# Performance work log

Hardware: AMD Instinct MI355X
Metric: run time of the kernel (lower is better)

Reference implementation:

```python
import jax, jax.numpy as jnp
import numpy as np

L = 5        # num_layers
D = 128      # emb_dim
H = 2 * D    # mlp hidden
N_ATOM_FEATS, ATOM_VOCAB = 9, 120
N_BOND_FEATS, BOND_VOCAB = 3, 6
BN_EPS = 1e-5


def setup_inputs() -> dict:
    key = jax.random.key(0)
    ks = jax.random.split(key, 16)
    N, E = 200000, 400000
    x = jax.random.randint(ks[0], (N, N_ATOM_FEATS), 0, ATOM_VOCAB)
    edge_index = jax.random.randint(ks[1], (2, E), 0, N)
    edge_attr = jax.random.randint(ks[2], (E, N_BOND_FEATS), 0, BOND_VOCAB)
    s = 0.02
    return {
        "x": x,
        "edge_index": edge_index,
        "edge_attr": edge_attr,
        "atom_emb": jax.random.normal(ks[3], (N_ATOM_FEATS, ATOM_VOCAB, D), jnp.float32) * s,
        "bond_emb": jax.random.normal(ks[4], (L, N_BOND_FEATS, BOND_VOCAB, D), jnp.float32) * s,
        "W1": jax.random.normal(ks[5], (L, D, H), jnp.float32) * s,
        "b1": jnp.zeros((L, H), jnp.float32),
        "bn1_g": jnp.ones((L, H), jnp.float32),
        "bn1_b": jnp.zeros((L, H), jnp.float32),
        "W2": jax.random.normal(ks[6], (L, H, D), jnp.float32) * s,
        "b2": jnp.zeros((L, D), jnp.float32),
        "eps": jnp.zeros((L,), jnp.float32),
        "out_bn_g": jnp.ones((L, D), jnp.float32),
        "out_bn_b": jnp.zeros((L, D), jnp.float32),
    }


def _batchnorm(z, g, b):
    mu = jnp.mean(z, axis=0, keepdims=True)
    var = jnp.var(z, axis=0, keepdims=True)
    return (z - mu) * jax.lax.rsqrt(var + BN_EPS) * g + b


def _multi_embed(tables, idx):
    # tables: [F, V, D], idx: [N, F] -> sum_f tables[f][idx[:, f]] : [N, D]
    gathered = jax.vmap(lambda tab, i: tab[i], in_axes=(0, 1))(tables, idx)  # [F, N, D]
    return jnp.sum(gathered, axis=0)


def reference(x, edge_index, edge_attr, atom_emb, bond_emb, W1, b1, bn1_g, bn1_b,
              W2, b2, eps, out_bn_g, out_bn_b):
    N = x.shape[0]
    src, dst = edge_index[0], edge_index[1]
    h = _multi_embed(atom_emb, x)  # AtomEncoder: [N, D]
    for l in range(L):
        e = _multi_embed(bond_emb[l], edge_attr)          # BondEncoder: [E, D]
        msg = jax.nn.relu(h[src] + e)                     # message
        aggr = jax.ops.segment_sum(msg, dst, num_segments=N)  # scatter-add
        z = (1.0 + eps[l]) * h + aggr                     # GIN combine
        z = jax.nn.relu(_batchnorm(z @ W1[l] + b1[l], bn1_g[l], bn1_b[l]))
        z = z @ W2[l] + b2[l]
        h = jax.nn.relu(_batchnorm(z, out_bn_g[l], out_bn_b[l]))  # relu+dropout(p=0)
    return h  # JK='last'
```

## Files before the change

kernel.cpp:

```cpp
#include <hip/hip_runtime.h>

#define NF_ATOM 9
#define NF_BOND 3
#define DD 128
#define HH 256
#define NLAYER 5
#define NSHARD 32
#define NCODE 216
#define GRAM_NB 256

typedef float fv4 __attribute__((ext_vector_type(4)));
typedef __bf16 bfv8 __attribute__((ext_vector_type(8)));
typedef unsigned int uv4 __attribute__((ext_vector_type(4)));

__device__ inline unsigned short f2bf(float f) {
    unsigned int u = __builtin_bit_cast(unsigned int, f);
    u = u + 0x7FFFu + ((u >> 16) & 1u);
    return (unsigned short)(u >> 16);
}
__device__ inline float bf2f(unsigned short s) {
    unsigned int u = ((unsigned int)s) << 16;
    return __builtin_bit_cast(float, u);
}

__global__ __launch_bounds__(256) void k_atom(const int* __restrict__ x,
        const float* __restrict__ emb, unsigned short* __restrict__ h, int N) {
    int gid = blockIdx.x * 256 + threadIdx.x;
    int n = gid >> 5;
    if (n >= N) return;
    int c = (gid & 31) << 2;
    const int* xr = x + n * NF_ATOM;
    float4 acc = make_float4(0.f, 0.f, 0.f, 0.f);
#pragma unroll
    for (int f = 0; f < NF_ATOM; ++f) {
        int idx = xr[f];
        float4 v = *(const float4*)(emb + ((size_t)(f * 120 + idx) * DD) + c);
        acc.x += v.x; acc.y += v.y; acc.z += v.z; acc.w += v.w;
    }
    ushort4 o;
    o.x = f2bf(acc.x); o.y = f2bf(acc.y); o.z = f2bf(acc.z); o.w = f2bf(acc.w);
    *(ushort4*)(h + (size_t)n * DD + c) = o;
}

__global__ __launch_bounds__(256) void k_wconv(const float* __restrict__ W1,
        const float* __restrict__ W2, unsigned short* __restrict__ W1t,
        unsigned short* __restrict__ W2t) {
    int id = blockIdx.x * 256 + threadIdx.x;
    const int T1 = NLAYER * 4 * 256 * 32;
    if (id < T1) {
        int k = id & 31, n = (id >> 5) & 255, kc = (id >> 13) & 3, l = id >> 15;
        int o = id & 32767;
        float w = W1[((size_t)(l * 128 + kc * 32 + k)) * 256 + n];
        unsigned short hi = f2bf(w);
        W1t[(size_t)l * 65536 + o] = hi;
        W1t[(size_t)l * 65536 + 32768 + o] = f2bf(w - bf2f(hi));
    } else {
        int id2 = id - T1;
        if (id2 >= NLAYER * 8 * 128 * 32) return;
        int k = id2 & 31, n = (id2 >> 5) & 127, kc = (id2 >> 12) & 7, l = id2 >> 15;
        int o = id2 & 32767;
        float w = W2[((size_t)(l * 256 + kc * 32 + k)) * 128 + n];
        unsigned short hi = f2bf(w);
        W2t[(size_t)l * 65536 + o] = hi;
        W2t[(size_t)l * 65536 + 32768 + o] = f2bf(w - bf2f(hi));
    }
}

__global__ __launch_bounds__(256) void k_bsumtab(const float* __restrict__ bemb,
        float* __restrict__ tab) {
    int id = blockIdx.x * 256 + threadIdx.x;
    if (id >= NLAYER * NCODE * DD) return;
    int c = id & 127;
    int code = (id >> 7) % NCODE;
    int l = id / (NCODE * DD);
    int a0 = code % 6, a1 = (code / 6) % 6, a2 = code / 36;
    const float* bl = bemb + (size_t)l * NF_BOND * 6 * DD;
    tab[id] = bl[(0 * 6 + a0) * DD + c] + bl[(1 * 6 + a1) * DD + c] + bl[(2 * 6 + a2) * DD + c];
}

__global__ __launch_bounds__(256) void k_deg(const int* __restrict__ ei, int* __restrict__ deg, int E) {
    int e = blockIdx.x * 256 + threadIdx.x;
    if (e < E) atomicAdd(&deg[ei[E + e]], 1);
}
__global__ __launch_bounds__(256) void k_bsum(const int* __restrict__ deg, int* __restrict__ bsum, int N) {
    __shared__ int red[256];
    int t = threadIdx.x, b = blockIdx.x;
    int i0 = b * 1024 + t * 4;
    int s = 0;
#pragma unroll
    for (int j = 0; j < 4; ++j) if (i0 + j < N) s += deg[i0 + j];
    red[t] = s; __syncthreads();
    for (int off = 128; off > 0; off >>= 1) {
        if (t < off) red[t] += red[t + off];
        __syncthreads();
    }
    if (t == 0) bsum[b] = red[0];
}
__global__ __launch_bounds__(256) void k_bscan(const int* __restrict__ bsum, int* __restrict__ boff, int nb) {
    __shared__ int ts[256];
    int t = threadIdx.x;
    int v = (t < nb) ? bsum[t] : 0;
    ts[t] = v; __syncthreads();
    for (int off = 1; off < 256; off <<= 1) {
        int u = (t >= off) ? ts[t - off] : 0;
        __syncthreads();
        ts[t] += u;
        __syncthreads();
    }
    if (t < nb) boff[t] = ts[t] - v;
}
__global__ __launch_bounds__(256) void k_csr(const int* deg, const int* __restrict__ boff,
        int* rs, int N, int E) {
    __shared__ int ts[256];
    int t = threadIdx.x, b = blockIdx.x;
    int i0 = b * 1024 + t * 4;
    int d[4];
#pragma unroll
    for (int j = 0; j < 4; ++j) d[j] = (i0 + j < N) ? deg[i0 + j] : 0;
    int tsum = d[0] + d[1] + d[2] + d[3];
    ts[t] = tsum; __syncthreads();
    for (int off = 1; off < 256; off <<= 1) {
        int u = (t >= off) ? ts[t - off] : 0;
        __syncthreads();
        ts[t] += u;
        __syncthreads();
    }
    int base = boff[b] + ts[t] - tsum;
    int p = 0;
#pragma unroll
    for (int j = 0; j < 4; ++j) {
        int dj = d[j];
        if (i0 + j < N) rs[i0 + j] = base + p;
        p += dj;
    }
    if (b == 0 && t == 0) rs[N] = E;
}
__global__ __launch_bounds__(256) void k_scatter(const int* __restrict__ ei,
        const int* __restrict__ ea, int* __restrict__ rs, int* __restrict__ epack, int E) {
    int e = blockIdx.x * 256 + threadIdx.x;
    if (e < E) {
        int pos = atomicAdd(&rs[ei[E + e]], 1);
        int code = ea[e * 3 + 0] + 6 * ea[e * 3 + 1] + 36 * ea[e * 3 + 2];
        epack[pos] = ei[e] | (code << 18);
    }
}

__global__ void k_red(const float* __restrict__ sh, int C, const float* __restrict__ bng,
        const float* __restrict__ bnb, float invN,
        float* __restrict__ sc_out, float* __restrict__ sh_out) {
    int t = threadIdx.x;
    if (t >= C) return;
    float a = 0.f, qq = 0.f;
#pragma unroll
    for (int s = 0; s < NSHARD; ++s) {
        a += sh[s * 2 * C + t];
        qq += sh[s * 2 * C + C + t];
    }
    float mu = a * invN;
    float var = qq * invN - mu * mu;
    float r = rsqrtf(var + 1e-5f);
    float sc = bng[t] * r;
    sc_out[t] = sc; sh_out[t] = bnb[t] - mu * sc;
}

__device__ inline void edge_acc(ushort4 hv, float4 bv, float4 sc, float4 sh, int mode, float* ag) {
    float h0 = bf2f(hv.x), h1 = bf2f(hv.y), h2 = bf2f(hv.z), h3 = bf2f(hv.w);
    if (mode) {
        h0 = fmaxf(h0 * sc.x + sh.x, 0.f); h1 = fmaxf(h1 * sc.y + sh.y, 0.f);
        h2 = fmaxf(h2 * sc.z + sh.z, 0.f); h3 = fmaxf(h3 * sc.w + sh.w, 0.f);
    }
    ag[0] += fmaxf(h0 + bv.x, 0.f); ag[1] += fmaxf(h1 + bv.y, 0.f);
    ag[2] += fmaxf(h2 + bv.z, 0.f); ag[3] += fmaxf(h3 + bv.w, 0.f);
}

__global__ __launch_bounds__(256) void k_zbuild(const unsigned short* __restrict__ y2h,
        const int* __restrict__ rs, const int* __restrict__ epack,
        const float* __restrict__ btab, const float* __restrict__ sctab,
        const float* __restrict__ shtab, const float* __restrict__ epsv,
        int l, int mode, unsigned short* __restrict__ z, int N) {
    int gid = blockIdx.x * 256 + threadIdx.x;
    int n = gid >> 5;
    if (n >= N) return;
    int c = (gid & 31) << 2;
    float4 sc4 = make_float4(1.f, 1.f, 1.f, 1.f), sh4 = make_float4(0.f, 0.f, 0.f, 0.f);
    if (mode) { sc4 = *(const float4*)(sctab + c); sh4 = *(const float4*)(shtab + c); }
    int p0 = (n == 0) ? 0 : rs[n - 1];
    int p1 = rs[n];
    float ag[4] = {0.f, 0.f, 0.f, 0.f};
    int p = p0;
    for (; p + 2 <= p1; p += 2) {
        int rec0 = epack[p], rec1 = epack[p + 1];
        int s0 = rec0 & 0x3FFFF, s1 = rec1 & 0x3FFFF;
        int c0 = ((unsigned int)rec0) >> 18, c1 = ((unsigned int)rec1) >> 18;
        ushort4 h0 = *(const ushort4*)(y2h + (size_t)s0 * DD + c);
        ushort4 h1 = *(const ushort4*)(y2h + (size_t)s1 * DD + c);
        float4 b0 = *(const float4*)(btab + (size_t)c0 * DD + c);
        float4 b1 = *(const float4*)(btab + (size_t)c1 * DD + c);
        edge_acc(h0, b0, sc4, sh4, mode, ag);
        edge_acc(h1, b1, sc4, sh4, mode, ag);
    }
    if (p < p1) {
        int rec = epack[p];
        int s0 = rec & 0x3FFFF;
        int c0 = ((unsigned int)rec) >> 18;
        ushort4 h0 = *(const ushort4*)(y2h + (size_t)s0 * DD + c);
        float4 b0 = *(const float4*)(btab + (size_t)c0 * DD + c);
        edge_acc(h0, b0, sc4, sh4, mode, ag);
    }
    float ep = 1.0f + epsv[l];
    ushort4 sv = *(const ushort4*)(y2h + (size_t)n * DD + c);
    float hz[4] = {bf2f(sv.x), bf2f(sv.y), bf2f(sv.z), bf2f(sv.w)};
    if (mode) {
        hz[0] = fmaxf(hz[0] * sc4.x + sh4.x, 0.f);
        hz[1] = fmaxf(hz[1] * sc4.y + sh4.y, 0.f);
        hz[2] = fmaxf(hz[2] * sc4.z + sh4.z, 0.f);
        hz[3] = fmaxf(hz[3] * sc4.w + sh4.w, 0.f);
    }
    ushort4 o;
    o.x = f2bf(ep * hz[0] + ag[0]);
    o.y = f2bf(ep * hz[1] + ag[1]);
    o.z = f2bf(ep * hz[2] + ag[2]);
    o.w = f2bf(ep * hz[3] + ag[3]);
    *(ushort4*)(z + (size_t)n * DD + c) = o;
}

__global__ __launch_bounds__(256) void k_gram(const unsigned short* __restrict__ z,
        float* __restrict__ shardG, float* __restrict__ csS, int N) {
    __shared__ uv4 zT[128 * 8];
    int tid = threadIdx.x;
    int lane = tid & 63, wave = tid >> 6, lq = lane >> 4, lr = lane & 15;
    int cg = tid & 15;
    float cs[8] = {0, 0, 0, 0, 0, 0, 0, 0};
    fv4 acc[2][8];
#pragma unroll
    for (int ti = 0; ti < 2; ++ti)
#pragma unroll
        for (int tj = 0; tj < 8; ++tj) acc[ti][tj] = (fv4){0.f, 0.f, 0.f, 0.f};

    int ntile = N >> 6;
    for (int t = blockIdx.x; t < ntile; t += GRAM_NB) {
        const unsigned short* zt0 = z + ((size_t)t << 6) * DD;
        __syncthreads();
#pragma unroll
        for (int i = 0; i < 2; ++i) {
            int rp = i * 16 + (tid >> 4);
            int r0 = rp * 2;
            uv4 a = *(const uv4*)(zt0 + (size_t)r0 * DD + cg * 8);
            uv4 b = *(const uv4*)(zt0 + (size_t)(r0 + 1) * DD + cg * 8);
            int g = rp >> 2;
            int eo = rp & 3;
#pragma unroll
            for (int j = 0; j < 4; ++j) {
                unsigned int lo0 = a[j] & 0xFFFFu, hi0 = a[j] >> 16;
                unsigned int lo1 = b[j] & 0xFFFFu, hi1 = b[j] >> 16;
                cs[2 * j] += bf2f((unsigned short)lo0) + bf2f((unsigned short)lo1);
                cs[2 * j + 1] += bf2f((unsigned short)hi0) + bf2f((unsigned short)hi1);
                int ch0 = cg * 8 + 2 * j, ch1 = ch0 + 1;
                int s0 = ch0 * 8 + (g ^ ((ch0 ^ (ch0 >> 3)) & 7));
                int s1 = ch1 * 8 + (g ^ ((ch1 ^ (ch1 >> 3)) & 7));
                ((unsigned int*)zT)[s0 * 4 + eo] = lo0 | (lo1 << 16);
                ((unsigned int*)zT)[s1 * 4 + eo] = hi0 | (hi1 << 16);
            }
        }
        __syncthreads();
#pragma unroll
        for (int ks = 0; ks < 2; ++ks) {
            bfv8 af[2], bfr[8];
#pragma unroll
            for (int ti = 0; ti < 2; ++ti) {
                int ch = wave * 32 + ti * 16 + lr;
                af[ti] = __builtin_bit_cast(bfv8, zT[ch * 8 + ((ks * 4 + lq) ^ ((ch ^ (ch >> 3)) & 7))]);
            }
#pragma unroll
            for (int tj = 0; tj < 8; ++tj) {
                int ch = tj * 16 + lr;
                bfr[tj] = __builtin_bit_cast(bfv8, zT[ch * 8 + ((ks * 4 + lq) ^ ((ch ^ (ch >> 3)) & 7))]);
            }
#pragma unroll
            for (int ti = 0; ti < 2; ++ti)
#pragma unroll
                for (int tj = 0; tj < 8; ++tj)
                    acc[ti][tj] = __builtin_amdgcn_mfma_f32_16x16x32_bf16(af[ti], bfr[tj], acc[ti][tj], 0, 0, 0);
        }
    }
    float* gsh = shardG + (size_t)blockIdx.x * (DD * DD);
#pragma unroll
    for (int ti = 0; ti < 2; ++ti) {
        int gi = wave * 32 + ti * 16 + lq * 4;
#pragma unroll
        for (int tj = 0; tj < 8; ++tj) {
            int gj = tj * 16 + lr;
#pragma unroll
            for (int r = 0; r < 4; ++r)
                gsh[(size_t)(gi + r) * DD + gj] = acc[ti][tj][r];
        }
    }
    __syncthreads();
    float* red = (float*)zT;
#pragma unroll
    for (int j = 0; j < 8; ++j) red[tid * 8 + j] = cs[j];
    __syncthreads();
    if (tid < 128) {
        int cgg = tid >> 3, j = tid & 7;
        float a = 0.f;
#pragma unroll
        for (int k = 0; k < 16; ++k) a += red[(k * 16 + cgg) * 8 + j];
        csS[blockIdx.x * DD + cgg * 8 + j] = a;
    }
}

__global__ __launch_bounds__(256) void k_gred(const float* __restrict__ shardG,
        const float* __restrict__ csS, float* __restrict__ G, float* __restrict__ cs) {
    int idx = blockIdx.x * 256 + threadIdx.x;
    if (idx < DD * DD) {
        float a = 0.f;
#pragma unroll 8
        for (int s = 0; s < GRAM_NB; ++s) a += shardG[(size_t)s * DD * DD + idx];
        G[idx] = a;
    } else if (idx < DD * DD + DD) {
        int t = idx - DD * DD;
        float a = 0.f;
#pragma unroll 8
        for (int s = 0; s < GRAM_NB; ++s) a += csS[s * DD + t];
        cs[t] = a;
    }
}

__global__ __launch_bounds__(128) void k_redG(const float* __restrict__ G,
        const float* __restrict__ cs, const unsigned short* __restrict__ W1l,
        const float* __restrict__ b1, const float* __restrict__ bng,
        const float* __restrict__ bnb, float invN,
        float* __restrict__ sc_out, float* __restrict__ sh_out) {
    __shared__ float wv[128];
    __shared__ float redA[128], redB[128];
    int j = blockIdx.x;
    int t = threadIdx.x;
    int kc = t >> 5, kk = t & 31;
    int o = kc * 8192 + j * 32 + kk;
    float w_t = bf2f(W1l[o]) + bf2f(W1l[32768 + o]);
    wv[t] = w_t;
    __syncthreads();
    const float4* Gr = (const float4*)(G + (size_t)t * DD);
    float d = 0.f;
#pragma unroll
    for (int i = 0; i < 32; ++i) {
        float4 g4 = Gr[i];
        d += g4.x * wv[i * 4] + g4.y * wv[i * 4 + 1] + g4.z * wv[i * 4 + 2] + g4.w * wv[i * 4 + 3];
    }
    redA[t] = w_t * d;
    redB[t] = cs[t] * w_t;
    __syncthreads();
    for (int off = 64; off > 0; off >>= 1) {
        if (t < off) { redA[t] += redA[t + off]; redB[t] += redB[t + off]; }
        __syncthreads();
    }
    if (t == 0) {
        float bj = b1[j];
        float csw = redB[0];
        float mean = csw * invN + bj;
        float ey2 = redA[0] * invN + 2.f * bj * csw * invN + bj * bj;
        float var = ey2 - mean * mean;
        float r = rsqrtf(var + 1e-5f);
        float sc = bng[j] * r;
        sc_out[j] = sc;
        sh_out[j] = bnb[j] - mean * sc + bj * sc;
    }
}

__global__ __launch_bounds__(256) void k_fgemm(const unsigned short* __restrict__ z,
        const unsigned short* __restrict__ W1l, const unsigned short* __restrict__ W2l,
        const float* __restrict__ sc1, const float* __restrict__ sh1,
        const float* __restrict__ bias2,
        unsigned short* __restrict__ y2h, float* __restrict__ shard, int N) {
    __shared__ uv4 smem[3072];
    uv4* zt = smem;
    uv4* wt = smem + 1024;
    uv4* at = smem;
    uv4* wt2 = smem + 2048;
    int tid = threadIdx.x;
    int row0 = blockIdx.x * 64;
    int wave = tid >> 6, lane = tid & 63, lq = lane >> 4, lr = lane & 15;
    int rbase = tid >> 4, gz = tid & 15;

    uv4 zr[4];
#pragma unroll
    for (int i = 0; i < 4; ++i)
        zr[i] = *(const uv4*)(z + (size_t)(row0 + i * 16 + rbase) * DD + gz * 8);
    const uv4* w1src = (const uv4*)W1l;
    uv4 wrh[4], wrl[4];
#pragma unroll
    for (int i = 0; i < 4; ++i) {
        wrh[i] = w1src[i * 256 + tid];
        wrl[i] = w1src[4096 + i * 256 + tid];
    }
#pragma unroll
    for (int i = 0; i < 4; ++i) {
        int row = i * 16 + rbase;
        zt[row * 16 + (gz ^ (row & 15))] = zr[i];
    }

    fv4 acc1[4][4];
#pragma unroll
    for (int mc = 0; mc < 4; ++mc)
#pragma unroll
        for (int nr = 0; nr < 4; ++nr) acc1[mc][nr] = (fv4){0.f, 0.f, 0.f, 0.f};

    for (int kc = 0; kc < 4; ++kc) {
        __syncthreads();
#pragma unroll
        for (int i = 0; i < 4; ++i) {
            int g = i * 256 + tid;
            int wn = g >> 2, gw = g & 3;
            int slot = wn * 4 + (gw ^ ((wn >> 1) & 3));
            wt[slot] = wrh[i];
            wt[1024 + slot] = wrl[i];
        }
        __syncthreads();
        if (kc < 3) {
#pragma unroll
            for (int i = 0; i < 4; ++i) {
                wrh[i] = w1src[(size_t)(kc + 1) * 1024 + i * 256 + tid];
                wrl[i] = w1src[4096 + (size_t)(kc + 1) * 1024 + i * 256 + tid];
            }
        }
        bfv8 wfh[4], wfl[4], zf[4];
#pragma unroll
        for (int mc = 0; mc < 4; ++mc) {
            int col = wave * 64 + mc * 16 + lr;
            int slot = col * 4 + (lq ^ ((col >> 1) & 3));
            wfh[mc] = __builtin_bit_cast(bfv8, wt[slot]);
            wfl[mc] = __builtin_bit_cast(bfv8, wt[1024 + slot]);
        }
#pragma unroll
        for (int nr = 0; nr < 4; ++nr) {
            int row = nr * 16 + lr;
            zf[nr] = __builtin_bit_cast(bfv8, zt[row * 16 + ((kc * 4 + lq) ^ (row & 15))]);
        }
#pragma unroll
        for (int mc = 0; mc < 4; ++mc)
#pragma unroll
            for (int nr = 0; nr < 4; ++nr) {
                acc1[mc][nr] = __builtin_amdgcn_mfma_f32_16x16x32_bf16(wfh[mc], zf[nr], acc1[mc][nr], 0, 0, 0);
                acc1[mc][nr] = __builtin_amdgcn_mfma_f32_16x16x32_bf16(wfl[mc], zf[nr], acc1[mc][nr], 0, 0, 0);
            }
    }
    __syncthreads();

    const uv4* w2src = (const uv4*)W2l;
    uv4 wr2h[2], wr2l[2];
    wr2h[0] = w2src[tid]; wr2h[1] = w2src[256 + tid];
    wr2l[0] = w2src[4096 + tid]; wr2l[1] = w2src[4096 + 256 + tid];

#pragma unroll
    for (int mc = 0; mc < 4; ++mc) {
        int ycol0 = wave * 64 + mc * 16 + lq * 4;
        float4 s4 = *(const float4*)(sc1 + ycol0);
        float4 h4 = *(const float4*)(sh1 + ycol0);
        int gg = wave * 8 + mc * 2 + (lq >> 1);
#pragma unroll
        for (int nr = 0; nr < 4; ++nr) {
            int zrow = nr * 16 + lr;
            float v0 = fmaxf(acc1[mc][nr][0] * s4.x + h4.x, 0.f);
            float v1 = fmaxf(acc1[mc][nr][1] * s4.y + h4.y, 0.f);
            float v2 = fmaxf(acc1[mc][nr][2] * s4.z + h4.z, 0.f);
            float v3 = fmaxf(acc1[mc][nr][3] * s4.w + h4.w, 0.f);
            uint2 pk;
            pk.x = (unsigned int)f2bf(v0) | ((unsigned int)f2bf(v1) << 16);
            pk.y = (unsigned int)f2bf(v2) | ((unsigned int)f2bf(v3) << 16);
            int gs = gg ^ (zrow & 15);
            ((uint2*)at)[(zrow * 32 + gs) * 2 + (lq & 1)] = pk;
        }
    }

    fv4 acc2[4][2];
#pragma unroll
    for (int m = 0; m < 4; ++m) { acc2[m][0] = (fv4){0.f,0.f,0.f,0.f}; acc2[m][1] = (fv4){0.f,0.f,0.f,0.f}; }

    for (int kc = 0; kc < 8; ++kc) {
        __syncthreads();
        {
            int wn = tid >> 2, gw = tid & 3;
            int slot = wn * 4 + (gw ^ ((wn >> 1) & 3));
            wt2[slot] = wr2h[0];
            wt2[512 + slot] = wr2l[0];
            int g3 = 256 + tid, wn3 = g3 >> 2, gw3 = g3 & 3;
            int slot3 = wn3 * 4 + (gw3 ^ ((wn3 >> 1) & 3));
            wt2[slot3] = wr2h[1];
            wt2[512 + slot3] = wr2l[1];
        }
        __syncthreads();
        if (kc < 7) {
            wr2h[0] = w2src[(size_t)(kc + 1) * 512 + tid];
            wr2h[1] = w2src[(size_t)(kc + 1) * 512 + 256 + tid];
            wr2l[0] = w2src[4096 + (size_t)(kc + 1) * 512 + tid];
            wr2l[1] = w2src[4096 + (size_t)(kc + 1) * 512 + 256 + tid];
        }
        bfv8 a[4], bh[2], bl[2];
#pragma unroll
        for (int m = 0; m < 4; ++m) {
            int row = m * 16 + lr;
            a[m] = __builtin_bit_cast(bfv8, at[row * 32 + ((kc * 4 + lq) ^ (row & 15))]);
        }
#pragma unroll
        for (int nb = 0; nb < 2; ++nb) {
            int col = wave * 32 + nb * 16 + lr;
            int slot = col * 4 + (lq ^ ((col >> 1) & 3));
            bh[nb] = __builtin_bit_cast(bfv8, wt2[slot]);
            bl[nb] = __builtin_bit_cast(bfv8, wt2[512 + slot]);
        }
#pragma unroll
        for (int m = 0; m < 4; ++m)
#pragma unroll
            for (int nb = 0; nb < 2; ++nb) {
                acc2[m][nb] = __builtin_amdgcn_mfma_f32_16x16x32_bf16(a[m], bh[nb], acc2[m][nb], 0, 0, 0);
                acc2[m][nb] = __builtin_amdgcn_mfma_f32_16x16x32_bf16(a[m], bl[nb], acc2[m][nb], 0, 0, 0);
            }
    }

    float bv[2], s[2], q[2];
#pragma unroll
    for (int nb = 0; nb < 2; ++nb) {
        bv[nb] = bias2[wave * 32 + nb * 16 + lr];
        s[nb] = 0.f; q[nb] = 0.f;
    }
#pragma unroll
    for (int m = 0; m < 4; ++m)
#pragma unroll
        for (int nb = 0; nb < 2; ++nb) {
            int col = wave * 32 + nb * 16 + lr;
#pragma unroll
            for (int r = 0; r < 4; ++r) {
                float v = acc2[m][nb][r] + bv[nb];
                unsigned short ub = f2bf(v);
                float vr = bf2f(ub);
                int row = row0 + m * 16 + lq * 4 + r;
                y2h[(size_t)row * DD + col] = ub;
                s[nb] += vr; q[nb] += vr * vr;
            }
        }
#pragma unroll
    for (int nb = 0; nb < 2; ++nb) {
        s[nb] += __shfl_xor(s[nb], 16); s[nb] += __shfl_xor(s[nb], 32);
        q[nb] += __shfl_xor(q[nb], 16); q[nb] += __shfl_xor(q[nb], 32);
    }
    if (lane < 16) {
        int shb = (blockIdx.x & (NSHARD - 1)) * 256;
#pragma unroll
        for (int nb = 0; nb < 2; ++nb) {
            int col = wave * 32 + nb * 16 + lr;
            atomicAdd(shard + shb + col, s[nb]);
            atomicAdd(shard + shb + 128 + col, q[nb]);
        }
    }
}

__global__ __launch_bounds__(256) void k_bnfinal(const unsigned short* __restrict__ y2h,
        const float* __restrict__ sc2, const float* __restrict__ sh2,
        float* __restrict__ out, int N) {
    size_t base = ((size_t)blockIdx.x * 256 + threadIdx.x) * 4;
    if (base >= (size_t)N * DD) return;
    int c = (int)(base & (DD - 1));
    ushort4 v = *(const ushort4*)(y2h + base);
    float4 s = *(const float4*)(sc2 + c);
    float4 t = *(const float4*)(sh2 + c);
    float4 o;
    o.x = fmaxf(bf2f(v.x) * s.x + t.x, 0.f);
    o.y = fmaxf(bf2f(v.y) * s.y + t.y, 0.f);
    o.z = fmaxf(bf2f(v.z) * s.z + t.z, 0.f);
    o.w = fmaxf(bf2f(v.w) * s.w + t.w, 0.f);
    *(float4*)(out + base) = o;
}

extern "C" void kernel_launch(void* const* d_in, const int* in_sizes, int n_in,
                              void* d_out, int out_size, void* d_ws, size_t ws_size,
                              hipStream_t stream) {
    const int* x = (const int*)d_in[0];
    const int* ei = (const int*)d_in[1];
    const int* ea = (const int*)d_in[2];
    const float* atom_emb = (const float*)d_in[3];
    const float* bond_emb = (const float*)d_in[4];
    const float* W1 = (const float*)d_in[5];
    const float* b1 = (const float*)d_in[6];
    const float* bn1_g = (const float*)d_in[7];
    const float* bn1_b = (const float*)d_in[8];
    const float* W2 = (const float*)d_in[9];
    const float* b2 = (const float*)d_in[10];
    const float* epsv = (const float*)d_in[11];
    const float* obn_g = (const float*)d_in[12];
    const float* obn_b = (const float*)d_in[13];
    int N = in_sizes[0] / NF_ATOM;
    int E = in_sizes[1] / 2;

    char* wsb = (char*)d_ws;
    unsigned short* y2h = (unsigned short*)wsb;
    unsigned short* zb = (unsigned short*)(wsb + (size_t)N * 256);
    int* epack = (int*)(wsb + (size_t)N * 512);
    unsigned short* w1t = (unsigned short*)(wsb + (size_t)N * 512 + (size_t)E * 4);
    unsigned short* w2t = w1t + 327680;
    float* btab = (float*)((char*)w2t + 655360);
    float* sc1 = btab + NLAYER * NCODE * DD;
    float* sh1 = sc1 + 256;
    float* sc2 = sh1 + 256;
    float* sh2 = sc2 + 128;
    float* G = sh2 + 128;
    float* cs = G + DD * DD;
    float* shardG = cs + DD;
    float* csS = shardG + (size_t)GRAM_NB * DD * DD;
    float* shard2 = csS + GRAM_NB * DD;
    size_t zero_f = (size_t)NLAYER * NSHARD * 256;
    int* rsarr = (int*)(shard2 + (size_t)NLAYER * NSHARD * 256);
    int* bsum = rsarr + (N + 1);
    int* boff = bsum + 256;
    float invN = 1.0f / (float)N;
    int nbk = (N + 1023) / 1024;

    k_wconv<<<1280, 256, 0, stream>>>(W1, W2, w1t, w2t);
    k_bsumtab<<<(NLAYER * NCODE * DD + 255) / 256, 256, 0, stream>>>(bond_emb, btab);
    hipMemsetAsync(rsarr, 0, ((size_t)N + 1) * 4, stream);
    hipMemsetAsync(shard2, 0, zero_f * sizeof(float), stream);
    k_deg<<<(E + 255) / 256, 256, 0, stream>>>(ei, rsarr, E);
    k_bsum<<<nbk, 256, 0, stream>>>(rsarr, bsum, N);
    k_bscan<<<1, 256, 0, stream>>>(bsum, boff, nbk);
    k_csr<<<nbk, 256, 0, stream>>>(rsarr, boff, rsarr, N, E);
    k_scatter<<<(E + 255) / 256, 256, 0, stream>>>(ei, ea, rsarr, epack, E);
    k_atom<<<(N * 32 + 255) / 256, 256, 0, stream>>>(x, atom_emb, y2h, N);

    int gb = N / 64;
    for (int l = 0; l < NLAYER; ++l) {
        float* sh2d = shard2 + (size_t)l * NSHARD * 256;
        k_zbuild<<<(N * 32 + 255) / 256, 256, 0, stream>>>(y2h, rsarr, epack,
                btab + (size_t)l * NCODE * DD, sc2, sh2, epsv, l, (l == 0) ? 0 : 1, zb, N);
        k_gram<<<GRAM_NB, 256, 0, stream>>>(zb, shardG, csS, N);
        k_gred<<<(DD * DD + DD + 255) / 256, 256, 0, stream>>>(shardG, csS, G, cs);
        k_redG<<<HH, 128, 0, stream>>>(G, cs, w1t + (size_t)l * 65536, b1 + l * HH,
                bn1_g + l * HH, bn1_b + l * HH, invN, sc1, sh1);
        k_fgemm<<<gb, 256, 0, stream>>>(zb, w1t + (size_t)l * 65536, w2t + (size_t)l * 65536,
                sc1, sh1, b2 + l * DD, y2h, sh2d, N);
        k_red<<<1, 128, 0, stream>>>(sh2d, 128, obn_g + l * DD, obn_b + l * DD, invN, sc2, sh2);
    }
    k_bnfinal<<<(int)(((size_t)N * DD / 4 + 255) / 256), 256, 0, stream>>>(
            y2h, sc2, sh2, (float*)d_out, N);
}
```

Measured before the change: 929.1 us.

## Make weight tiles wave-private in fused MLP GEMM to drop block barriers

Each wave now loads and stages in shared memory only the slice of W1/W2 columns it consumes. This removes the two __syncthreads per K-chunk in both GEMM loops, leaving one barrier before each loop. The wave writes the next chunk's weights into its private LDS region after its MFMAs, with a compiler memory fence between them. The risk is a missing intra-wave ordering guarantee between the LDS reads and the later overwrite, and a possible change in LDS bank-conflict behaviour.

```diff
diff --git a/kernel.cpp b/kernel.cpp
--- a/kernel.cpp
+++ b/kernel.cpp
@@ -374,9 +374,11 @@
         unsigned short* __restrict__ y2h, float* __restrict__ shard, int N) {
     __shared__ uv4 smem[3072];
     uv4* zt = smem;
-    uv4* wt = smem + 1024;
+    uv4* wtH = smem + 1024;
+    uv4* wtL = smem + 2048;
     uv4* at = smem;
-    uv4* wt2 = smem + 2048;
+    uv4* wt2H = smem + 2048;
+    uv4* wt2L = smem + 2560;
     int tid = threadIdx.x;
     int row0 = blockIdx.x * 64;
     int wave = tid >> 6, lane = tid & 63, lq = lane >> 4, lr = lane & 15;
@@ -390,14 +392,24 @@
     uv4 wrh[4], wrl[4];
 #pragma unroll
     for (int i = 0; i < 4; ++i) {
-        wrh[i] = w1src[i * 256 + tid];
-        wrl[i] = w1src[4096 + i * 256 + tid];
+        int gloc = i * 64 + lane;
+        wrh[i] = w1src[wave * 256 + gloc];
+        wrl[i] = w1src[4096 + wave * 256 + gloc];
     }
 #pragma unroll
     for (int i = 0; i < 4; ++i) {
         int row = i * 16 + rbase;
         zt[row * 16 + (gz ^ (row & 15))] = zr[i];
     }
+#pragma unroll
+    for (int i = 0; i < 4; ++i) {
+        int gloc = i * 64 + lane;
+        int lc = gloc >> 2, gw = gloc & 3;
+        int slot = wave * 256 + lc * 4 + (gw ^ ((lc >> 1) & 3));
+        wtH[slot] = wrh[i];
+        wtL[slot] = wrl[i];
+    }
+    __syncthreads();
 
     fv4 acc1[4][4];
 #pragma unroll
@@ -406,30 +418,21 @@
         for (int nr = 0; nr < 4; ++nr) acc1[mc][nr] = (fv4){0.f, 0.f, 0.f, 0.f};
 
     for (int kc = 0; kc < 4; ++kc) {
-        __syncthreads();
-#pragma unroll
-        for (int i = 0; i < 4; ++i) {
-            int g = i * 256 + tid;
-            int wn = g >> 2, gw = g & 3;
-            int slot = wn * 4 + (gw ^ ((wn >> 1) & 3));
-            wt[slot] = wrh[i];
-            wt[1024 + slot] = wrl[i];
-        }
-        __syncthreads();
         if (kc < 3) {
 #pragma unroll
             for (int i = 0; i < 4; ++i) {
-                wrh[i] = w1src[(size_t)(kc + 1) * 1024 + i * 256 + tid];
-                wrl[i] = w1src[4096 + (size_t)(kc + 1) * 1024 + i * 256 + tid];
+                int gloc = i * 64 + lane;
+                wrh[i] = w1src[(size_t)(kc + 1) * 1024 + wave * 256 + gloc];
+                wrl[i] = w1src[4096 + (size_t)(kc + 1) * 1024 + wave * 256 + gloc];
             }
         }
         bfv8 wfh[4], wfl[4], zf[4];
 #pragma unroll
         for (int mc = 0; mc < 4; ++mc) {
-            int col = wave * 64 + mc * 16 + lr;
-            int slot = col * 4 + (lq ^ ((col >> 1) & 3));
-            wfh[mc] = __builtin_bit_cast(bfv8, wt[slot]);
-            wfl[mc] = __builtin_bit_cast(bfv8, wt[1024 + slot]);
+            int lc = mc * 16 + lr;
+            int slot = wave * 256 + lc * 4 + (lq ^ ((lc >> 1) & 3));
+            wfh[mc] = __builtin_bit_cast(bfv8, wtH[slot]);
+            wfl[mc] = __builtin_bit_cast(bfv8, wtL[slot]);
         }
 #pragma unroll
         for (int nr = 0; nr < 4; ++nr) {
@@ -443,13 +446,28 @@
                 acc1[mc][nr] = __builtin_amdgcn_mfma_f32_16x16x32_bf16(wfh[mc], zf[nr], acc1[mc][nr], 0, 0, 0);
                 acc1[mc][nr] = __builtin_amdgcn_mfma_f32_16x16x32_bf16(wfl[mc], zf[nr], acc1[mc][nr], 0, 0, 0);
             }
+        asm volatile("" ::: "memory");
+        if (kc < 3) {
+#pragma unroll
+            for (int i = 0; i < 4; ++i) {
+                int gloc = i * 64 + lane;
+                int lc = gloc >> 2, gw = gloc & 3;
+                int slot = wave * 256 + lc * 4 + (gw ^ ((lc >> 1) & 3));
+                wtH[slot] = wrh[i];
+                wtL[slot] = wrl[i];
+            }
+        }
     }
     __syncthreads();
 
     const uv4* w2src = (const uv4*)W2l;
     uv4 wr2h[2], wr2l[2];
-    wr2h[0] = w2src[tid]; wr2h[1] = w2src[256 + tid];
-    wr2l[0] = w2src[4096 + tid]; wr2l[1] = w2src[4096 + 256 + tid];
+#pragma unroll
+    for (int i = 0; i < 2; ++i) {
+        int gloc = i * 64 + lane;
+        wr2h[i] = w2src[wave * 128 + gloc];
+        wr2l[i] = w2src[4096 + wave * 128 + gloc];
+    }
 
 #pragma unroll
     for (int mc = 0; mc < 4; ++mc) {
@@ -471,29 +489,28 @@
             ((uint2*)at)[(zrow * 32 + gs) * 2 + (lq & 1)] = pk;
         }
     }
+#pragma unroll
+    for (int i = 0; i < 2; ++i) {
+        int gloc = i * 64 + lane;
+        int lc = gloc >> 2, gw = gloc & 3;
+        int slot = wave * 128 + lc * 4 + (gw ^ ((lc >> 1) & 3));
+        wt2H[slot] = wr2h[i];
+        wt2L[slot] = wr2l[i];
+    }
+    __syncthreads();
 
     fv4 acc2[4][2];
 #pragma unroll
     for (int m = 0; m < 4; ++m) { acc2[m][0] = (fv4){0.f,0.f,0.f,0.f}; acc2[m][1] = (fv4){0.f,0.f,0.f,0.f}; }
 
     for (int kc = 0; kc < 8; ++kc) {
-        __syncthreads();
-        {
-            int wn = tid >> 2, gw = tid & 3;
-            int slot = wn * 4 + (gw ^ ((wn >> 1) & 3));
-            wt2[slot] = wr2h[0];
-            wt2[512 + slot] = wr2l[0];
-            int g3 = 256 + tid, wn3 = g3 >> 2, gw3 = g3 & 3;
-            int slot3 = wn3 * 4 + (gw3 ^ ((wn3 >> 1) & 3));
-            wt2[slot3] = wr2h[1];
-            wt2[512 + slot3] = wr2l[1];
-        }
-        __syncthreads();
         if (kc < 7) {
-            wr2h[0] = w2src[(size_t)(kc + 1) * 512 + tid];
-            wr2h[1] = w2src[(size_t)(kc + 1) * 512 + 256 + tid];
-            wr2l[0] = w2src[4096 + (size_t)(kc + 1) * 512 + tid];
-            wr2l[1] = w2src[4096 + (size_t)(kc + 1) * 512 + 256 + tid];
+#pragma unroll
+            for (int i = 0; i < 2; ++i) {
+                int gloc = i * 64 + lane;
+                wr2h[i] = w2src[(size_t)(kc + 1) * 512 + wave * 128 + gloc];
+                wr2l[i] = w2src[4096 + (size_t)(kc + 1) * 512 + wave * 128 + gloc];
+            }
         }
         bfv8 a[4], bh[2], bl[2];
 #pragma unroll
@@ -503,10 +520,10 @@
         }
 #pragma unroll
         for (int nb = 0; nb < 2; ++nb) {
-            int col = wave * 32 + nb * 16 + lr;
-            int slot = col * 4 + (lq ^ ((col >> 1) & 3));
-            bh[nb] = __builtin_bit_cast(bfv8, wt2[slot]);
-            bl[nb] = __builtin_bit_cast(bfv8, wt2[512 + slot]);
+            int lc = nb * 16 + lr;
+            int slot = wave * 128 + lc * 4 + (lq ^ ((lc >> 1) & 3));
+            bh[nb] = __builtin_bit_cast(bfv8, wt2H[slot]);
+            bl[nb] = __builtin_bit_cast(bfv8, wt2L[slot]);
         }
 #pragma unroll
         for (int m = 0; m < 4; ++m)
@@ -515,6 +532,17 @@
                 acc2[m][nb] = __builtin_amdgcn_mfma_f32_16x16x32_bf16(a[m], bh[nb], acc2[m][nb], 0, 0, 0);
                 acc2[m][nb] = __builtin_amdgcn_mfma_f32_16x16x32_bf16(a[m], bl[nb], acc2[m][nb], 0, 0, 0);
             }
+        asm volatile("" ::: "memory");
+        if (kc < 7) {
+#pragma unroll
+            for (int i = 0; i < 2; ++i) {
+                int gloc = i * 64 + lane;
+                int lc = gloc >> 2, gw = gloc & 3;
+                int slot = wave * 128 + lc * 4 + (gw ^ ((lc >> 1) & 3));
+                wt2H[slot] = wr2h[i];
+                wt2L[slot] = wr2l[i];
+            }
+        }
     }
 
     float bv[2], s[2], q[2];
```

New measurement: 904.3 us. 1.03x faster.

## Load GEMM weight fragments directly from global into registers, dropping LDS staging

Applied to the files above, without the earlier changes.

The fused MLP GEMM kernel no longer stages W1/W2 tiles through shared memory. Each lane now loads its MFMA weight fragment straight from global memory (L2-resident weights) into double-buffered registers, which removes the per-k-chunk LDS writes and two barriers per iteration. Shared memory per block drops from 48KB to 32KB and launch bounds request 3 blocks per CU to raise occupancy. The cost is redundant global/L2 weight traffic across blocks and waves, plus more register pressure from the double buffers.

```diff
diff --git a/kernel.cpp b/kernel.cpp
--- a/kernel.cpp
+++ b/kernel.cpp
@@ -367,16 +367,14 @@
     }
 }
 
-__global__ __launch_bounds__(256) void k_fgemm(const unsigned short* __restrict__ z,
+__global__ __launch_bounds__(256, 3) void k_fgemm(const unsigned short* __restrict__ z,
         const unsigned short* __restrict__ W1l, const unsigned short* __restrict__ W2l,
         const float* __restrict__ sc1, const float* __restrict__ sh1,
         const float* __restrict__ bias2,
         unsigned short* __restrict__ y2h, float* __restrict__ shard, int N) {
-    __shared__ uv4 smem[3072];
+    __shared__ uv4 smem[2048];
     uv4* zt = smem;
-    uv4* wt = smem + 1024;
     uv4* at = smem;
-    uv4* wt2 = smem + 2048;
     int tid = threadIdx.x;
     int row0 = blockIdx.x * 64;
     int wave = tid >> 6, lane = tid & 63, lq = lane >> 4, lr = lane & 15;
@@ -387,17 +385,19 @@
     for (int i = 0; i < 4; ++i)
         zr[i] = *(const uv4*)(z + (size_t)(row0 + i * 16 + rbase) * DD + gz * 8);
     const uv4* w1src = (const uv4*)W1l;
-    uv4 wrh[4], wrl[4];
-#pragma unroll
-    for (int i = 0; i < 4; ++i) {
-        wrh[i] = w1src[i * 256 + tid];
-        wrl[i] = w1src[4096 + i * 256 + tid];
+    uv4 wh[2][4], wl[2][4];
+#pragma unroll
+    for (int mc = 0; mc < 4; ++mc) {
+        int col = wave * 64 + mc * 16 + lr;
+        wh[0][mc] = w1src[(size_t)col * 4 + lq];
+        wl[0][mc] = w1src[4096 + (size_t)col * 4 + lq];
     }
 #pragma unroll
     for (int i = 0; i < 4; ++i) {
         int row = i * 16 + rbase;
         zt[row * 16 + (gz ^ (row & 15))] = zr[i];
     }
+    __syncthreads();
 
     fv4 acc1[4][4];
 #pragma unroll
@@ -405,32 +405,18 @@
 #pragma unroll
         for (int nr = 0; nr < 4; ++nr) acc1[mc][nr] = (fv4){0.f, 0.f, 0.f, 0.f};
 
+#pragma unroll
     for (int kc = 0; kc < 4; ++kc) {
-        __syncthreads();
-#pragma unroll
-        for (int i = 0; i < 4; ++i) {
-            int g = i * 256 + tid;
-            int wn = g >> 2, gw = g & 3;
-            int slot = wn * 4 + (gw ^ ((wn >> 1) & 3));
-            wt[slot] = wrh[i];
-            wt[1024 + slot] = wrl[i];
-        }
-        __syncthreads();
+        const int cur = kc & 1, nxt = cur ^ 1;
         if (kc < 3) {
 #pragma unroll
-            for (int i = 0; i < 4; ++i) {
-                wrh[i] = w1src[(size_t)(kc + 1) * 1024 + i * 256 + tid];
-                wrl[i] = w1src[4096 + (size_t)(kc + 1) * 1024 + i * 256 + tid];
-            }
-        }
-        bfv8 wfh[4], wfl[4], zf[4];
-#pragma unroll
-        for (int mc = 0; mc < 4; ++mc) {
-            int col = wave * 64 + mc * 16 + lr;
-            int slot = col * 4 + (lq ^ ((col >> 1) & 3));
-            wfh[mc] = __builtin_bit_cast(bfv8, wt[slot]);
-            wfl[mc] = __builtin_bit_cast(bfv8, wt[1024 + slot]);
-        }
+            for (int mc = 0; mc < 4; ++mc) {
+                int col = wave * 64 + mc * 16 + lr;
+                wh[nxt][mc] = w1src[(size_t)((kc + 1) * 256 + col) * 4 + lq];
+                wl[nxt][mc] = w1src[4096 + (size_t)((kc + 1) * 256 + col) * 4 + lq];
+            }
+        }
+        bfv8 zf[4];
 #pragma unroll
         for (int nr = 0; nr < 4; ++nr) {
             int row = nr * 16 + lr;
@@ -440,16 +426,22 @@
         for (int mc = 0; mc < 4; ++mc)
 #pragma unroll
             for (int nr = 0; nr < 4; ++nr) {
-                acc1[mc][nr] = __builtin_amdgcn_mfma_f32_16x16x32_bf16(wfh[mc], zf[nr], acc1[mc][nr], 0, 0, 0);
-                acc1[mc][nr] = __builtin_amdgcn_mfma_f32_16x16x32_bf16(wfl[mc], zf[nr], acc1[mc][nr], 0, 0, 0);
+                acc1[mc][nr] = __builtin_amdgcn_mfma_f32_16x16x32_bf16(
+                        __builtin_bit_cast(bfv8, wh[cur][mc]), zf[nr], acc1[mc][nr], 0, 0, 0);
+                acc1[mc][nr] = __builtin_amdgcn_mfma_f32_16x16x32_bf16(
+                        __builtin_bit_cast(bfv8, wl[cur][mc]), zf[nr], acc1[mc][nr], 0, 0, 0);
             }
     }
     __syncthreads();
 
     const uv4* w2src = (const uv4*)W2l;
-    uv4 wr2h[2], wr2l[2];
-    wr2h[0] = w2src[tid]; wr2h[1] = w2src[256 + tid];
-    wr2l[0] = w2src[4096 + tid]; wr2l[1] = w2src[4096 + 256 + tid];
+    uv4 w2h[2][2], w2l[2][2];
+#pragma unroll
+    for (int nb = 0; nb < 2; ++nb) {
+        int col = wave * 32 + nb * 16 + lr;
+        w2h[0][nb] = w2src[(size_t)col * 4 + lq];
+        w2l[0][nb] = w2src[4096 + (size_t)col * 4 + lq];
+    }
 
 #pragma unroll
     for (int mc = 0; mc < 4; ++mc) {
@@ -471,49 +463,37 @@
             ((uint2*)at)[(zrow * 32 + gs) * 2 + (lq & 1)] = pk;
         }
     }
+    __syncthreads();
 
     fv4 acc2[4][2];
 #pragma unroll
     for (int m = 0; m < 4; ++m) { acc2[m][0] = (fv4){0.f,0.f,0.f,0.f}; acc2[m][1] = (fv4){0.f,0.f,0.f,0.f}; }
 
+#pragma unroll
     for (int kc = 0; kc < 8; ++kc) {
-        __syncthreads();
-        {
-            int wn = tid >> 2, gw = tid & 3;
-            int slot = wn * 4 + (gw ^ ((wn >> 1) & 3));
-            wt2[slot] = wr2h[0];
-            wt2[512 + slot] = wr2l[0];
-            int g3 = 256 + tid, wn3 = g3 >> 2, gw3 = g3 & 3;
-            int slot3 = wn3 * 4 + (gw3 ^ ((wn3 >> 1) & 3));
-            wt2[slot3] = wr2h[1];
-            wt2[512 + slot3] = wr2l[1];
-        }
-        __syncthreads();
+        const int cur = kc & 1, nxt = cur ^ 1;
         if (kc < 7) {
-            wr2h[0] = w2src[(size_t)(kc + 1) * 512 + tid];
-            wr2h[1] = w2src[(size_t)(kc + 1) * 512 + 256 + tid];
-            wr2l[0] = w2src[4096 + (size_t)(kc + 1) * 512 + tid];
-            wr2l[1] = w2src[4096 + (size_t)(kc + 1) * 512 + 256 + tid];
-        }
-        bfv8 a[4], bh[2], bl[2];
+#pragma unroll
+            for (int nb = 0; nb < 2; ++nb) {
+                int col = wave * 32 + nb * 16 + lr;
+                w2h[nxt][nb] = w2src[(size_t)((kc + 1) * 128 + col) * 4 + lq];
+                w2l[nxt][nb] = w2src[4096 + (size_t)((kc + 1) * 128 + col) * 4 + lq];
+            }
+        }
+        bfv8 a[4];
 #pragma unroll
         for (int m = 0; m < 4; ++m) {
             int row = m * 16 + lr;
             a[m] = __builtin_bit_cast(bfv8, at[row * 32 + ((kc * 4 + lq) ^ (row & 15))]);
         }
 #pragma unroll
-        for (int nb = 0; nb < 2; ++nb) {
-            int col = wave * 32 + nb * 16 + lr;
-            int slot = col * 4 + (lq ^ ((col >> 1) & 3));
-            bh[nb] = __builtin_bit_cast(bfv8, wt2[slot]);
-            bl[nb] = __builtin_bit_cast(bfv8, wt2[512 + slot]);
-        }
-#pragma unroll
         for (int m = 0; m < 4; ++m)
 #pragma unroll
             for (int nb = 0; nb < 2; ++nb) {
-                acc2[m][nb] = __builtin_amdgcn_mfma_f32_16x16x32_bf16(a[m], bh[nb], acc2[m][nb], 0, 0, 0);
-                acc2[m][nb] = __builtin_amdgcn_mfma_f32_16x16x32_bf16(a[m], bl[nb], acc2[m][nb], 0, 0, 0);
+                acc2[m][nb] = __builtin_amdgcn_mfma_f32_16x16x32_bf16(
+                        a[m], __builtin_bit_cast(bfv8, w2h[cur][nb]), acc2[m][nb], 0, 0, 0);
+                acc2[m][nb] = __builtin_amdgcn_mfma_f32_16x16x32_bf16(
+                        a[m], __builtin_bit_cast(bfv8, w2l[cur][nb]), acc2[m][nb], 0, 0, 0);
             }
     }
 
```

Result: faster. 896.1 us (-3.6%).
